# Kernel tuning notes

Measured on AMD Instinct MI355X. Metric: run time of the kernel, lower is better.

Reference implementation:

```python
import jax, jax.numpy as jnp
import numpy as np

N_BASIS = 8
CUTOFF = 5.0
NORM_FACTOR = 16.0


def setup_inputs() -> dict:
    key = jax.random.key(0)
    ks = jax.random.split(key, 10)
    N, E, C = 20000, 320000, 32
    s = 1.0 / np.sqrt(C)
    return {
        "node0": jax.random.normal(ks[0], (N, C), jnp.float32),
        "node1": jax.random.normal(ks[1], (N, C, 3), jnp.float32),
        "node2": jax.random.normal(ks[2], (N, C, 3, 3), jnp.float32),
        "rij": jax.random.normal(ks[3], (E, 3), jnp.float32) * 1.5,
        "Wrad": jax.random.normal(ks[4], (11, N_BASIS, C), jnp.float32) * 0.3,
        "U": jax.random.normal(ks[5], (3, C, C), jnp.float32) * s,
        "V": jax.random.normal(ks[6], (8, C, C), jnp.float32) * s,
        "Wg": jax.random.normal(ks[7], (3, C, C), jnp.float32) * s,
        "idx_i": jax.random.randint(ks[8], (E,), 0, N),
        "idx_j": jax.random.randint(ks[9], (E,), 0, N),
    }


def reference(node0, node1, node2, rij, Wrad, U, V, Wg, idx_i, idx_j):
    N, C = node0.shape
    # radial basis (Gaussian RBF * cosine cutoff envelope)
    dist = jnp.sqrt(jnp.sum(rij * rij, -1) + 1e-12)           # [E]
    rhat = rij / dist[:, None]                                 # [E,3]
    centers = jnp.linspace(0.5, CUTOFF, N_BASIS, dtype=node0.dtype)
    fc = 0.5 * (jnp.cos(jnp.pi * jnp.clip(dist / CUTOFF, 0.0, 1.0)) + 1.0)
    rbf = jnp.exp(-4.0 * (dist[:, None] - centers) ** 2) * fc[:, None]  # [E,B]
    # per-coupling-path radial filters: 11 paths (in_way, r_way, out_way)
    w = jnp.einsum('eb,pbc->pec', rbf, Wrad)                   # [11,E,C]
    # gather neighbor (node_j) features per edge
    g0 = node0[idx_j]                                          # [E,C]
    g1 = node1[idx_j]                                          # [E,C,3]
    g2 = node2[idx_j]                                          # [E,C,3,3]
    m1 = rhat                                                  # [E,3]
    m2 = rhat[:, :, None] * rhat[:, None, :]                   # [E,3,3]
    # graph conv: contract node_j tensor with r-way moment, weighted by radial filter
    # paths: 0:(0,0,0) 1:(0,1,1) 2:(0,2,2) 3:(1,0,1) 4:(1,1,0) 5:(1,1,2)
    #        6:(1,2,1) 7:(2,0,2) 8:(2,1,1) 9:(2,2,0) 10:(2,2,2)
    msg0 = (g0 * w[0]
            + jnp.einsum('eca,ea->ec', g1, m1) * w[4]
            + jnp.einsum('ecab,eab->ec', g2, m2) * w[9])
    msg1 = (jnp.einsum('ec,ea->eca', g0 * w[1], m1)
            + g1 * w[3][:, :, None]
            + jnp.einsum('eca,eab->ecb', g1, m2) * w[6][:, :, None]
            + jnp.einsum('ecab,eb->eca', g2, m1) * w[8][:, :, None])
    msg2 = (jnp.einsum('ec,eab->ecab', g0 * w[2], m2)
            + jnp.einsum('eca,eb->ecab', g1 * w[5][:, :, None], m1)
            + g2 * w[7][:, :, None, None]
            + jnp.einsum('ecab,ebd->ecad', g2, m2) * w[10][:, :, None, None])
    # scatter_add aggregation into per-atom features, normalized
    a0 = jax.ops.segment_sum(msg0, idx_i, num_segments=N) / NORM_FACTOR
    a1 = jax.ops.segment_sum(msg1, idx_i, num_segments=N) / NORM_FACTOR
    a2 = jax.ops.segment_sum(msg2, idx_i, num_segments=N) / NORM_FACTOR
    # multi-body self-interaction (2-body linear U + 3-body products V)
    y0 = (jnp.einsum('nc,cd->nd', a0, U[0])
          + jnp.einsum('nc,cd->nd', a0 * a0, V[0])
          + jnp.einsum('nc,cd->nd', jnp.einsum('nca,nca->nc', a1, a1), V[3])
          + jnp.einsum('nc,cd->nd', jnp.einsum('ncab,ncab->nc', a2, a2), V[6]))
    y1 = (jnp.einsum('nca,cd->nda', a1, U[1])
          + jnp.einsum('nca,cd->nda', a0[:, :, None] * a1, V[1])
          + jnp.einsum('nca,cd->nda', jnp.einsum('nca,ncab->ncb', a1, a2), V[5]))
    y2 = (jnp.einsum('ncab,cd->ndab', a2, U[2])
          + jnp.einsum('ncab,cd->ndab', a0[:, :, None, None] * a2, V[2])
          + jnp.einsum('ncab,cd->ndab', a1[:, :, :, None] * a1[:, :, None, :], V[4])
          + jnp.einsum('ncab,cd->ndab', jnp.einsum('ncab,ncbd->ncad', a2, a2), V[7]))
    # gated nonlinearity (scalar channel gates tensor ways) + residual add
    new0 = node0 + jax.nn.silu(y0 @ Wg[0])
    new1 = node1 + y1 * jax.nn.silu(y0 @ Wg[1])[:, :, None]
    new2 = node2 + y2 * jax.nn.silu(y0 @ Wg[2])[:, :, None, None]
    return (new0, new1, new2)
```

## Files before the change

### kernel.cpp

```cpp
#include <hip/hip_runtime.h>
#include <hip/hip_fp16.h>

#define NCH 32
#define NB 8
#define NPB 8

typedef __attribute__((ext_vector_type(2))) _Float16 half2r;

__device__ __forceinline__ unsigned short f2h(float f) {
    return __half_as_ushort(__float2half_rn(f));
}
__device__ __forceinline__ float h2f_lo(unsigned int u) {
    half2r v = __builtin_bit_cast(half2r, u);
    return (float)v.x;
}
__device__ __forceinline__ float h2f_hi(unsigned int u) {
    half2r v = __builtin_bit_cast(half2r, u);
    return (float)v.y;
}

__device__ __forceinline__ float fdot2u(unsigned int a, unsigned int b, float c) {
#if __has_builtin(__builtin_amdgcn_fdot2)
    return __builtin_amdgcn_fdot2(__builtin_bit_cast(half2r, a),
                                  __builtin_bit_cast(half2r, b), c, false);
#else
    half2r av = __builtin_bit_cast(half2r, a);
    half2r bv = __builtin_bit_cast(half2r, b);
    return c + (float)av.x * (float)bv.x + (float)av.y * (float)bv.y;
#endif
}

__device__ __forceinline__ void acc8h(float& y, uint4 w, uint4 f) {
    y = fdot2u(w.x, f.x, y);
    y = fdot2u(w.y, f.y, y);
    y = fdot2u(w.z, f.z, y);
    y = fdot2u(w.w, f.w, y);
}
__device__ __forceinline__ void acc8fh(float& y, uint4 w, float4 a, float4 b) {
    y += h2f_lo(w.x) * a.x + h2f_hi(w.x) * a.y + h2f_lo(w.y) * a.z + h2f_hi(w.y) * a.w
       + h2f_lo(w.z) * b.x + h2f_hi(w.z) * b.y + h2f_lo(w.w) * b.z + h2f_hi(w.w) * b.w;
}

__global__ __launch_bounds__(256) void wprep_kernel(
    const float* __restrict__ U, const float* __restrict__ V,
    const float* __restrict__ Wg, const float* __restrict__ Wrad,
    unsigned short* __restrict__ wswz, unsigned int* __restrict__ wradp)
{
    int idx = blockIdx.x * 256 + threadIdx.x;
    if (idx < 14 * 1024) {
        int m = idx >> 10, r = idx & 1023;
        int c = r >> 5, d = r & 31;
        float v;
        if (m < 3)       v = U[m * 1024 + c * 32 + d];
        else if (m < 11) v = V[(m - 3) * 1024 + c * 32 + d];
        else             v = Wg[(m - 11) * 1024 + c * 32 + d];
        wswz[m * 1024 + (c >> 3) * 256 + d * 8 + (c & 7)] = f2h(v);
    } else {
        int k = idx - 14 * 1024;
        if (k < 11 * 4 * 32) {
            int c = k & 31, bb = (k >> 5) & 3, p = k >> 7;
            float lo = Wrad[p * 256 + (2 * bb) * 32 + c] * (1.0f / 16.0f);
            float hi = Wrad[p * 256 + (2 * bb + 1) * 32 + c] * (1.0f / 16.0f);
            wradp[(p * 4 + bb) * 32 + c] =
                (unsigned int)f2h(lo) | ((unsigned int)f2h(hi) << 16);
        }
    }
}

__global__ __launch_bounds__(256) void hist_kernel(
    const int* __restrict__ idx_i, int* __restrict__ counts, int E)
{
    int e = blockIdx.x * 256 + threadIdx.x;
    if (e < E) atomicAdd(&counts[idx_i[e]], 1);
}

__global__ __launch_bounds__(256) void scan_reduce_kernel(
    const int* __restrict__ counts, int* __restrict__ blocksums, int N)
{
    const int tid = threadIdx.x;
    const int base = blockIdx.x * 1024;
    int v = 0;
    #pragma unroll
    for (int k = 0; k < 4; ++k) {
        int i = base + tid * 4 + k;
        if (i < N) v += counts[i];
    }
    #pragma unroll
    for (int off = 1; off < 64; off <<= 1) v += __shfl_xor(v, off, 64);
    __shared__ int wsum[4];
    if ((tid & 63) == 0) wsum[tid >> 6] = v;
    __syncthreads();
    if (tid == 0) blocksums[blockIdx.x] = wsum[0] + wsum[1] + wsum[2] + wsum[3];
}

__global__ void scan_top_kernel(
    const int* __restrict__ blocksums, int* __restrict__ bases,
    int* __restrict__ offsets, int nb, int N)
{
    int l = threadIdx.x;
    int v = (l < nb) ? blocksums[l] : 0;
    int incl = v;
    #pragma unroll
    for (int off = 1; off < 64; off <<= 1) {
        int t = __shfl_up(incl, off, 64);
        if (l >= off) incl += t;
    }
    if (l < nb) bases[l] = incl - v;
    if (l == nb - 1) offsets[N] = incl;
}

__global__ __launch_bounds__(256) void scan_write_kernel(
    int* __restrict__ cursor, const int* __restrict__ bases,
    int* __restrict__ offsets, int N)
{
    const int tid = threadIdx.x;
    const int i0 = blockIdx.x * 1024 + tid * 4;
    int v[4]; int lsum = 0;
    #pragma unroll
    for (int k = 0; k < 4; ++k) {
        int i = i0 + k;
        v[k] = (i < N) ? cursor[i] : 0;
        lsum += v[k];
    }
    int incl = lsum;
    #pragma unroll
    for (int off = 1; off < 64; off <<= 1) {
        int t = __shfl_up(incl, off, 64);
        if ((tid & 63) >= off) incl += t;
    }
    __shared__ int wsum[4];
    if ((tid & 63) == 63) wsum[tid >> 6] = incl;
    __syncthreads();
    int add = bases[blockIdx.x];
    for (int w = 0; w < (tid >> 6); ++w) add += wsum[w];
    int run = add + incl - lsum;
    #pragma unroll
    for (int k = 0; k < 4; ++k) {
        int i = i0 + k;
        if (i < N) { offsets[i] = run; cursor[i] = run; run += v[k]; }
    }
}

__global__ __launch_bounds__(256) void scatter_meta_kernel(
    const int* __restrict__ idx_i, const int* __restrict__ idx_j,
    const float* __restrict__ rij, int* __restrict__ cursor,
    int* __restrict__ jord, float4* __restrict__ meta2, int E)
{
    int e = blockIdx.x * 256 + threadIdx.x;
    if (e >= E) return;
    float rx = rij[3 * e + 0], ry = rij[3 * e + 1], rz = rij[3 * e + 2];
    float dist = sqrtf(rx * rx + ry * ry + rz * rz + 1e-12f);
    float inv = 1.0f / dist;
    float tcl = fminf(dist * 0.2f, 1.0f);
    float fc = 0.5f * (cosf(3.14159265358979f * tcl) + 1.0f);
    float rbf[NB];
    #pragma unroll
    for (int b = 0; b < NB; ++b) {
        float dd = dist - (0.5f + (float)b * (4.5f / 7.0f));
        rbf[b] = expf(-4.0f * dd * dd) * fc;
    }
    unsigned int rb01 = (unsigned int)f2h(rbf[0]) | ((unsigned int)f2h(rbf[1]) << 16);
    unsigned int rb23 = (unsigned int)f2h(rbf[2]) | ((unsigned int)f2h(rbf[3]) << 16);
    unsigned int rb45 = (unsigned int)f2h(rbf[4]) | ((unsigned int)f2h(rbf[5]) << 16);
    unsigned int rb67 = (unsigned int)f2h(rbf[6]) | ((unsigned int)f2h(rbf[7]) << 16);
    int slot = atomicAdd(&cursor[idx_i[e]], 1);
    jord[slot] = idx_j[e];
    meta2[2 * slot + 0] = make_float4(rx * inv, ry * inv, rz * inv, __uint_as_float(rb01));
    meta2[2 * slot + 1] = make_float4(__uint_as_float(rb23), __uint_as_float(rb45),
                                      __uint_as_float(rb67), 0.0f);
}

__global__ __launch_bounds__(256) void transpose_nodes_kernel(
    const float* __restrict__ node0, const float* __restrict__ node1,
    const float* __restrict__ node2, unsigned short* __restrict__ n0h,
    unsigned short* __restrict__ n1h, unsigned short* __restrict__ n2h, int N)
{
    int n = blockIdx.x * 8 + (threadIdx.x >> 5);
    int c = threadIdx.x & 31;
    if (n >= N) return;
    n0h[n * 32 + c] = f2h(node0[n * 32 + c]);
    #pragma unroll
    for (int a = 0; a < 3; ++a) n1h[n * 96 + a * 32 + c] = f2h(node1[n * 96 + c * 3 + a]);
    #pragma unroll
    for (int k = 0; k < 9; ++k) n2h[n * 288 + k * 32 + c] = f2h(node2[n * 288 + c * 9 + k]);
}

__global__ __launch_bounds__(256, 4) void aggregate_kernel(
    const unsigned short* __restrict__ n0h, const unsigned short* __restrict__ n1h,
    const unsigned short* __restrict__ n2h, const unsigned int* __restrict__ wradp,
    const int* __restrict__ jord, const float4* __restrict__ meta2,
    const int* __restrict__ offsets,
    float* __restrict__ a0, float* __restrict__ a1, float* __restrict__ a2,
    int N)
{
    const int c = threadIdx.x & 31;
    const int g = threadIdx.x >> 5;
    const int n = blockIdx.x * NPB + g;
    if (n >= N) return;

    unsigned int wr[11][4];
    #pragma unroll
    for (int p = 0; p < 11; ++p)
        #pragma unroll
        for (int bb = 0; bb < 4; ++bb)
            wr[p][bb] = wradp[(p * 4 + bb) * 32 + c];

    const int beg = offsets[n], end = offsets[n + 1];

    float A0 = 0.f;
    float A1[3] = {0.f, 0.f, 0.f};
    float A2[9] = {0.f, 0.f, 0.f, 0.f, 0.f, 0.f, 0.f, 0.f, 0.f};

    float4 M0n = make_float4(0.f, 0.f, 0.f, 0.f), M1n = M0n;
    unsigned short G0n = 0, G1n[3] = {0, 0, 0}, G2n[9] = {};

    int s = beg;
    if (s < end) {
        int j = jord[s];
        M0n = meta2[2 * s + 0]; M1n = meta2[2 * s + 1];
        G0n = n0h[j * 32 + c];
        #pragma unroll
        for (int a = 0; a < 3; ++a) G1n[a] = n1h[j * 96 + a * 32 + c];
        #pragma unroll
        for (int k = 0; k < 9; ++k) G2n[k] = n2h[j * 288 + k * 32 + c];
    }

    while (s < end) {
        float4 M0 = M0n, M1 = M1n;
        float G0 = __half2float(__ushort_as_half(G0n));
        float G1[3], G2[9];
        #pragma unroll
        for (int a = 0; a < 3; ++a) G1[a] = __half2float(__ushort_as_half(G1n[a]));
        #pragma unroll
        for (int k = 0; k < 9; ++k) G2[k] = __half2float(__ushort_as_half(G2n[k]));

        int sn = s + 1;
        if (sn < end) {
            int j = jord[sn];
            M0n = meta2[2 * sn + 0]; M1n = meta2[2 * sn + 1];
            G0n = n0h[j * 32 + c];
            #pragma unroll
            for (int a = 0; a < 3; ++a) G1n[a] = n1h[j * 96 + a * 32 + c];
            #pragma unroll
            for (int k = 0; k < 9; ++k) G2n[k] = n2h[j * 288 + k * 32 + c];
        }

        float h[3] = { M0.x, M0.y, M0.z };
        unsigned int rb01 = __float_as_uint(M0.w);
        unsigned int rb23 = __float_as_uint(M1.x);
        unsigned int rb45 = __float_as_uint(M1.y);
        unsigned int rb67 = __float_as_uint(M1.z);

        float w[11];
        #pragma unroll
        for (int p = 0; p < 11; ++p)
            w[p] = fdot2u(rb01, wr[p][0],
                   fdot2u(rb23, wr[p][1],
                   fdot2u(rb45, wr[p][2],
                   fdot2u(rb67, wr[p][3], 0.0f))));

        float s1 = G1[0] * h[0] + G1[1] * h[1] + G1[2] * h[2];
        float tt[3];
        #pragma unroll
        for (int a = 0; a < 3; ++a)
            tt[a] = G2[a * 3 + 0] * h[0] + G2[a * 3 + 1] * h[1] + G2[a * 3 + 2] * h[2];
        float s2 = tt[0] * h[0] + tt[1] * h[1] + tt[2] * h[2];

        A0 += G0 * w[0] + s1 * w[4] + s2 * w[9];
        #pragma unroll
        for (int a = 0; a < 3; ++a)
            A1[a] += (G0 * w[1] + s1 * w[6]) * h[a] + G1[a] * w[3] + tt[a] * w[8];
        #pragma unroll
        for (int a = 0; a < 3; ++a) {
            float pre = G0 * w[2] * h[a] + G1[a] * w[5] + tt[a] * w[10];
            #pragma unroll
            for (int b = 0; b < 3; ++b)
                A2[a * 3 + b] += pre * h[b] + G2[a * 3 + b] * w[7];
        }
        s = sn;
    }

    a0[n * 32 + c] = A0;
    #pragma unroll
    for (int a = 0; a < 3; ++a) a1[n * 96 + a * 32 + c] = A1[a];
    #pragma unroll
    for (int k = 0; k < 9; ++k) a2[n * 288 + k * 32 + c] = A2[k];
}

__global__ __launch_bounds__(256) void node_kernel(
    const float* __restrict__ node0, const float* __restrict__ node1,
    const float* __restrict__ node2, const unsigned short* __restrict__ wswz,
    float* __restrict__ out0, float* __restrict__ out1, float* __restrict__ out2,
    int N)
{
    __shared__ alignas(16) unsigned short wT[14 * 1024];
    __shared__ alignas(16) unsigned short feat[NPB * 49 * 32];
    __shared__ alignas(16) float y0s[NPB][32];

    {
        const uint4* src = reinterpret_cast<const uint4*>(wswz);
        uint4* dst = reinterpret_cast<uint4*>(wT);
        for (int i = threadIdx.x; i < 14 * 128; i += 256) dst[i] = src[i];
    }

    const int g = threadIdx.x >> 5;
    const int lane = threadIdx.x & 31;
    const int n = blockIdx.x * NPB + g;
    const bool active = (n < N);

    if (active) {
        const int c = lane;
        float A0 = out0[n * 32 + c];
        float A1[3], A2[9];
        #pragma unroll
        for (int a = 0; a < 3; ++a) A1[a] = out1[n * 96 + a * 32 + c];
        #pragma unroll
        for (int k = 0; k < 9; ++k) A2[k] = out2[n * 288 + k * 32 + c];

        unsigned short* F = &feat[g * 49 * 32];
        F[0 * 32 + c] = f2h(A0);
        F[1 * 32 + c] = f2h(A0 * A0);
        F[2 * 32 + c] = f2h(A1[0] * A1[0] + A1[1] * A1[1] + A1[2] * A1[2]);
        float n2 = 0.f;
        #pragma unroll
        for (int k = 0; k < 9; ++k) n2 += A2[k] * A2[k];
        F[3 * 32 + c] = f2h(n2);
        #pragma unroll
        for (int a = 0; a < 3; ++a) {
            F[(4 + a) * 32 + c] = f2h(A1[a]);
            F[(7 + a) * 32 + c] = f2h(A0 * A1[a]);
        }
        #pragma unroll
        for (int b = 0; b < 3; ++b) {
            float s = A1[0] * A2[0 * 3 + b] + A1[1] * A2[1 * 3 + b] + A1[2] * A2[2 * 3 + b];
            F[(10 + b) * 32 + c] = f2h(s);
        }
        #pragma unroll
        for (int k = 0; k < 9; ++k) {
            F[(13 + k) * 32 + c] = f2h(A2[k]);
            F[(22 + k) * 32 + c] = f2h(A0 * A2[k]);
        }
        #pragma unroll
        for (int a = 0; a < 3; ++a)
            #pragma unroll
            for (int b = 0; b < 3; ++b)
                F[(31 + a * 3 + b) * 32 + c] = f2h(A1[a] * A1[b]);
        #pragma unroll
        for (int a = 0; a < 3; ++a)
            #pragma unroll
            for (int dd = 0; dd < 3; ++dd) {
                float s = A2[a * 3 + 0] * A2[0 * 3 + dd] + A2[a * 3 + 1] * A2[1 * 3 + dd]
                        + A2[a * 3 + 2] * A2[2 * 3 + dd];
                F[(40 + a * 3 + dd) * 32 + c] = f2h(s);
            }
    }
    __syncthreads();

    const int d = lane;
    float y0v = 0.f;
    float y1v[3] = {0.f, 0.f, 0.f};
    float y2v[9] = {0.f, 0.f, 0.f, 0.f, 0.f, 0.f, 0.f, 0.f, 0.f};

    if (active) {
        const uint4* W4 = reinterpret_cast<const uint4*>(wT);
        const uint4* F4 = reinterpret_cast<const uint4*>(&feat[g * 49 * 32]);
        for (int q = 0; q < 4; ++q) {
            const int q32d = q * 32 + d;
            acc8h(y0v, W4[0 * 128 + q32d], F4[0 * 4 + q]);
            acc8h(y0v, W4[3 * 128 + q32d], F4[1 * 4 + q]);
            acc8h(y0v, W4[6 * 128 + q32d], F4[2 * 4 + q]);
            acc8h(y0v, W4[9 * 128 + q32d], F4[3 * 4 + q]);
            uint4 wU1 = W4[1 * 128 + q32d];
            uint4 wV1 = W4[4 * 128 + q32d];
            uint4 wV5 = W4[8 * 128 + q32d];
            #pragma unroll
            for (int a = 0; a < 3; ++a) {
                acc8h(y1v[a], wU1, F4[(4 + a) * 4 + q]);
                acc8h(y1v[a], wV1, F4[(7 + a) * 4 + q]);
                acc8h(y1v[a], wV5, F4[(10 + a) * 4 + q]);
            }
            uint4 wU2 = W4[2 * 128 + q32d];
            uint4 wV2 = W4[5 * 128 + q32d];
            uint4 wV4 = W4[7 * 128 + q32d];
            uint4 wV7 = W4[10 * 128 + q32d];
            #pragma unroll
            for (int k = 0; k < 9; ++k) {
                acc8h(y2v[k], wU2, F4[(13 + k) * 4 + q]);
                acc8h(y2v[k], wV2, F4[(22 + k) * 4 + q]);
                acc8h(y2v[k], wV4, F4[(31 + k) * 4 + q]);
                acc8h(y2v[k], wV7, F4[(40 + k) * 4 + q]);
            }
        }
        y0s[g][d] = y0v;
    }
    __syncthreads();

    if (!active) return;

    float t0 = 0.f, t1 = 0.f, t2 = 0.f;
    {
        const uint4* W4 = reinterpret_cast<const uint4*>(wT);
        const float4* Y4 = reinterpret_cast<const float4*>(y0s[g]);
        #pragma unroll
        for (int q = 0; q < 4; ++q) {
            const int q32d = q * 32 + d;
            float4 ya = Y4[2 * q], yb = Y4[2 * q + 1];
            acc8fh(t0, W4[11 * 128 + q32d], ya, yb);
            acc8fh(t1, W4[12 * 128 + q32d], ya, yb);
            acc8fh(t2, W4[13 * 128 + q32d], ya, yb);
        }
    }
    float s0 = t0 / (1.0f + expf(-t0));
    float s1 = t1 / (1.0f + expf(-t1));
    float s2 = t2 / (1.0f + expf(-t2));

    out0[n * 32 + d] = node0[n * 32 + d] + s0;
    #pragma unroll
    for (int a = 0; a < 3; ++a)
        out1[n * 96 + d * 3 + a] = node1[n * 96 + d * 3 + a] + y1v[a] * s1;
    #pragma unroll
    for (int k = 0; k < 9; ++k)
        out2[n * 288 + d * 9 + k] = node2[n * 288 + d * 9 + k] + y2v[k] * s2;
}

extern "C" void kernel_launch(void* const* d_in, const int* in_sizes, int n_in,
                              void* d_out, int out_size, void* d_ws, size_t ws_size,
                              hipStream_t stream)
{
    const float* node0 = (const float*)d_in[0];
    const float* node1 = (const float*)d_in[1];
    const float* node2 = (const float*)d_in[2];
    const float* rij   = (const float*)d_in[3];
    const float* Wrad  = (const float*)d_in[4];
    const float* U     = (const float*)d_in[5];
    const float* V     = (const float*)d_in[6];
    const float* Wg    = (const float*)d_in[7];
    const int* idx_i   = (const int*)d_in[8];
    const int* idx_j   = (const int*)d_in[9];

    const int N = in_sizes[0] / 32;
    const int E = in_sizes[3] / 3;

    float* out0 = (float*)d_out;
    float* out1 = out0 + (size_t)N * 32;
    float* out2 = out1 + (size_t)N * 96;

    size_t off = 0;
    auto walloc = [&](size_t bytes) -> void* {
        off = (off + 63) & ~(size_t)63;
        void* p = (char*)d_ws + off;
        off += bytes;
        return p;
    };
    int*    cursor    = (int*)   walloc((size_t)N * 4);
    int*    offsets   = (int*)   walloc((size_t)(N + 1) * 4);
    int*    blocksums = (int*)   walloc(64 * 4);
    int*    bases     = (int*)   walloc(64 * 4);
    int*    jord      = (int*)   walloc((size_t)E * 4);
    float4* meta2     = (float4*)walloc((size_t)E * 2 * sizeof(float4));
    unsigned short* n0h = (unsigned short*)walloc((size_t)N * 32 * 2);
    unsigned short* n1h = (unsigned short*)walloc((size_t)N * 96 * 2);
    unsigned short* n2h = (unsigned short*)walloc((size_t)N * 288 * 2);
    unsigned short* wswz = (unsigned short*)walloc(14 * 1024 * 2);
    unsigned int*  wradp = (unsigned int*)walloc(11 * 4 * 32 * 4);
    (void)ws_size;

    const int nb = (N + 1023) / 1024;

    hipMemsetAsync(cursor, 0, (size_t)N * sizeof(int), stream);

    wprep_kernel<<<dim3((14 * 1024 + 11 * 4 * 32 + 255) / 256), dim3(256), 0, stream>>>(
        U, V, Wg, Wrad, wswz, wradp);
    hist_kernel<<<dim3((E + 255) / 256), dim3(256), 0, stream>>>(idx_i, cursor, E);
    scan_reduce_kernel<<<dim3(nb), dim3(256), 0, stream>>>(cursor, blocksums, N);
    scan_top_kernel<<<dim3(1), dim3(64), 0, stream>>>(blocksums, bases, offsets, nb, N);
    scan_write_kernel<<<dim3(nb), dim3(256), 0, stream>>>(cursor, bases, offsets, N);
    scatter_meta_kernel<<<dim3((E + 255) / 256), dim3(256), 0, stream>>>(
        idx_i, idx_j, rij, cursor, jord, meta2, E);
    transpose_nodes_kernel<<<dim3((N + 7) / 8), dim3(256), 0, stream>>>(
        node0, node1, node2, n0h, n1h, n2h, N);

    aggregate_kernel<<<dim3((N + NPB - 1) / NPB), dim3(256), 0, stream>>>(
        n0h, n1h, n2h, wradp, jord, meta2, offsets, out0, out1, out2, N);

    node_kernel<<<dim3((N + NPB - 1) / NPB), dim3(256), 0, stream>>>(
        node0, node1, node2, wswz, out0, out1, out2, N);
}
```

Baseline: 285.2 us.

## Pack per-node fp16 features into 32-byte records, single-block scan, smaller aggregate blocks

Node features are packed per (node, channel) into one contiguous 32-byte record of 13 fp16 values plus padding. The gather in the aggregation loop therefore becomes two 16-byte vector loads instead of thirteen scattered 2-byte loads. The three-kernel prefix scan is merged into one 1024-thread single-block kernel, which removes two launches. The aggregate kernel now runs 64-thread blocks covering two nodes each, which should improve load balance across uneven degrees. The padding adds about 23% more bytes per gathered row, and the serial per-thread scan loop is a small latency cost.

```diff
diff --git a/kernel.cpp b/kernel.cpp
--- a/kernel.cpp
+++ b/kernel.cpp
@@ -74,71 +74,41 @@
     if (e < E) atomicAdd(&counts[idx_i[e]], 1);
 }
 
-__global__ __launch_bounds__(256) void scan_reduce_kernel(
-    const int* __restrict__ counts, int* __restrict__ blocksums, int N)
+__global__ __launch_bounds__(1024) void scan_kernel(
+    int* __restrict__ cursor ,
+    int* __restrict__ offsets, int N)
 {
     const int tid = threadIdx.x;
-    const int base = blockIdx.x * 1024;
-    int v = 0;
-    #pragma unroll
-    for (int k = 0; k < 4; ++k) {
-        int i = base + tid * 4 + k;
-        if (i < N) v += counts[i];
-    }
-    #pragma unroll
-    for (int off = 1; off < 64; off <<= 1) v += __shfl_xor(v, off, 64);
-    __shared__ int wsum[4];
-    if ((tid & 63) == 0) wsum[tid >> 6] = v;
-    __syncthreads();
-    if (tid == 0) blocksums[blockIdx.x] = wsum[0] + wsum[1] + wsum[2] + wsum[3];
-}
-
-__global__ void scan_top_kernel(
-    const int* __restrict__ blocksums, int* __restrict__ bases,
-    int* __restrict__ offsets, int nb, int N)
-{
-    int l = threadIdx.x;
-    int v = (l < nb) ? blocksums[l] : 0;
-    int incl = v;
+    const int lane = tid & 63, wid = tid >> 6;
+    const int per = (N + 1023) / 1024;
+    const int i0 = tid * per;
+    const int i1 = min(i0 + per, N);
+
+    int lsum = 0;
+    for (int i = i0; i < i1; ++i) lsum += cursor[i];
+
+    int incl = lsum;
     #pragma unroll
     for (int off = 1; off < 64; off <<= 1) {
         int t = __shfl_up(incl, off, 64);
-        if (l >= off) incl += t;
-    }
-    if (l < nb) bases[l] = incl - v;
-    if (l == nb - 1) offsets[N] = incl;
-}
-
-__global__ __launch_bounds__(256) void scan_write_kernel(
-    int* __restrict__ cursor, const int* __restrict__ bases,
-    int* __restrict__ offsets, int N)
-{
-    const int tid = threadIdx.x;
-    const int i0 = blockIdx.x * 1024 + tid * 4;
-    int v[4]; int lsum = 0;
-    #pragma unroll
-    for (int k = 0; k < 4; ++k) {
-        int i = i0 + k;
-        v[k] = (i < N) ? cursor[i] : 0;
-        lsum += v[k];
-    }
-    int incl = lsum;
-    #pragma unroll
-    for (int off = 1; off < 64; off <<= 1) {
-        int t = __shfl_up(incl, off, 64);
-        if ((tid & 63) >= off) incl += t;
-    }
-    __shared__ int wsum[4];
-    if ((tid & 63) == 63) wsum[tid >> 6] = incl;
+        if (lane >= off) incl += t;
+    }
+    __shared__ int wsums[16], wbase[16];
+    if (lane == 63) wsums[wid] = incl;
     __syncthreads();
-    int add = bases[blockIdx.x];
-    for (int w = 0; w < (tid >> 6); ++w) add += wsum[w];
-    int run = add + incl - lsum;
-    #pragma unroll
-    for (int k = 0; k < 4; ++k) {
-        int i = i0 + k;
-        if (i < N) { offsets[i] = run; cursor[i] = run; run += v[k]; }
-    }
+    if (tid == 0) {
+        int acc = 0;
+        #pragma unroll
+        for (int k = 0; k < 16; ++k) { int t = wsums[k]; wbase[k] = acc; acc += t; }
+    }
+    __syncthreads();
+
+    int run = wbase[wid] + incl - lsum;
+    for (int i = i0; i < i1; ++i) {
+        int cv = cursor[i];
+        offsets[i] = run; cursor[i] = run; run += cv;
+    }
+    if (tid == 1023) offsets[N] = wbase[15] + incl;
 }
 
 __global__ __launch_bounds__(256) void scatter_meta_kernel(
@@ -170,24 +140,31 @@
                                       __uint_as_float(rb67), 0.0f);
 }
 
-__global__ __launch_bounds__(256) void transpose_nodes_kernel(
+__global__ __launch_bounds__(256) void pack_nodes_kernel(
     const float* __restrict__ node0, const float* __restrict__ node1,
-    const float* __restrict__ node2, unsigned short* __restrict__ n0h,
-    unsigned short* __restrict__ n1h, unsigned short* __restrict__ n2h, int N)
+    const float* __restrict__ node2, uint4* __restrict__ pk, int N)
 {
     int n = blockIdx.x * 8 + (threadIdx.x >> 5);
     int c = threadIdx.x & 31;
     if (n >= N) return;
-    n0h[n * 32 + c] = f2h(node0[n * 32 + c]);
-    #pragma unroll
-    for (int a = 0; a < 3; ++a) n1h[n * 96 + a * 32 + c] = f2h(node1[n * 96 + c * 3 + a]);
-    #pragma unroll
-    for (int k = 0; k < 9; ++k) n2h[n * 288 + k * 32 + c] = f2h(node2[n * 288 + c * 9 + k]);
-}
-
-__global__ __launch_bounds__(256, 4) void aggregate_kernel(
-    const unsigned short* __restrict__ n0h, const unsigned short* __restrict__ n1h,
-    const unsigned short* __restrict__ n2h, const unsigned int* __restrict__ wradp,
+    unsigned short r[16];
+    r[0] = f2h(node0[n * 32 + c]);
+    #pragma unroll
+    for (int a = 0; a < 3; ++a) r[1 + a] = f2h(node1[n * 96 + c * 3 + a]);
+    #pragma unroll
+    for (int k = 0; k < 9; ++k) r[4 + k] = f2h(node2[n * 288 + c * 9 + k]);
+    r[13] = r[14] = r[15] = 0;
+    unsigned int u[8];
+    #pragma unroll
+    for (int i = 0; i < 8; ++i)
+        u[i] = (unsigned int)r[2 * i] | ((unsigned int)r[2 * i + 1] << 16);
+    uint4* dst = pk + (size_t)n * 64 + c * 2;
+    dst[0] = make_uint4(u[0], u[1], u[2], u[3]);
+    dst[1] = make_uint4(u[4], u[5], u[6], u[7]);
+}
+
+__global__ __launch_bounds__(64) void aggregate_kernel(
+    const uint4* __restrict__ pk, const unsigned int* __restrict__ wradp,
     const int* __restrict__ jord, const float4* __restrict__ meta2,
     const int* __restrict__ offsets,
     float* __restrict__ a0, float* __restrict__ a1, float* __restrict__ a2,
@@ -195,7 +172,7 @@
 {
     const int c = threadIdx.x & 31;
     const int g = threadIdx.x >> 5;
-    const int n = blockIdx.x * NPB + g;
+    const int n = blockIdx.x * 2 + g;
     if (n >= N) return;
 
     unsigned int wr[11][4];
@@ -212,38 +189,33 @@
     float A2[9] = {0.f, 0.f, 0.f, 0.f, 0.f, 0.f, 0.f, 0.f, 0.f};
 
     float4 M0n = make_float4(0.f, 0.f, 0.f, 0.f), M1n = M0n;
-    unsigned short G0n = 0, G1n[3] = {0, 0, 0}, G2n[9] = {};
+    uint4 Q0n = make_uint4(0, 0, 0, 0), Q1n = Q0n;
 
     int s = beg;
     if (s < end) {
         int j = jord[s];
         M0n = meta2[2 * s + 0]; M1n = meta2[2 * s + 1];
-        G0n = n0h[j * 32 + c];
-        #pragma unroll
-        for (int a = 0; a < 3; ++a) G1n[a] = n1h[j * 96 + a * 32 + c];
-        #pragma unroll
-        for (int k = 0; k < 9; ++k) G2n[k] = n2h[j * 288 + k * 32 + c];
+        const uint4* P = pk + (size_t)j * 64 + c * 2;
+        Q0n = P[0]; Q1n = P[1];
     }
 
     while (s < end) {
         float4 M0 = M0n, M1 = M1n;
-        float G0 = __half2float(__ushort_as_half(G0n));
-        float G1[3], G2[9];
-        #pragma unroll
-        for (int a = 0; a < 3; ++a) G1[a] = __half2float(__ushort_as_half(G1n[a]));
-        #pragma unroll
-        for (int k = 0; k < 9; ++k) G2[k] = __half2float(__ushort_as_half(G2n[k]));
+        uint4 Q0 = Q0n, Q1 = Q1n;
 
         int sn = s + 1;
         if (sn < end) {
             int j = jord[sn];
             M0n = meta2[2 * sn + 0]; M1n = meta2[2 * sn + 1];
-            G0n = n0h[j * 32 + c];
-            #pragma unroll
-            for (int a = 0; a < 3; ++a) G1n[a] = n1h[j * 96 + a * 32 + c];
-            #pragma unroll
-            for (int k = 0; k < 9; ++k) G2n[k] = n2h[j * 288 + k * 32 + c];
-        }
+            const uint4* P = pk + (size_t)j * 64 + c * 2;
+            Q0n = P[0]; Q1n = P[1];
+        }
+
+        float G0    = h2f_lo(Q0.x);
+        float G1[3] = { h2f_hi(Q0.x), h2f_lo(Q0.y), h2f_hi(Q0.y) };
+        float G2[9] = { h2f_lo(Q0.z), h2f_hi(Q0.z), h2f_lo(Q0.w), h2f_hi(Q0.w),
+                        h2f_lo(Q1.x), h2f_hi(Q1.x), h2f_lo(Q1.y), h2f_hi(Q1.y),
+                        h2f_lo(Q1.z) };
 
         float h[3] = { M0.x, M0.y, M0.z };
         unsigned int rb01 = __float_as_uint(M0.w);
@@ -454,34 +426,26 @@
     };
     int*    cursor    = (int*)   walloc((size_t)N * 4);
     int*    offsets   = (int*)   walloc((size_t)(N + 1) * 4);
-    int*    blocksums = (int*)   walloc(64 * 4);
-    int*    bases     = (int*)   walloc(64 * 4);
     int*    jord      = (int*)   walloc((size_t)E * 4);
     float4* meta2     = (float4*)walloc((size_t)E * 2 * sizeof(float4));
-    unsigned short* n0h = (unsigned short*)walloc((size_t)N * 32 * 2);
-    unsigned short* n1h = (unsigned short*)walloc((size_t)N * 96 * 2);
-    unsigned short* n2h = (unsigned short*)walloc((size_t)N * 288 * 2);
+    uint4*  pk        = (uint4*) walloc((size_t)N * 1024);
     unsigned short* wswz = (unsigned short*)walloc(14 * 1024 * 2);
     unsigned int*  wradp = (unsigned int*)walloc(11 * 4 * 32 * 4);
     (void)ws_size;
 
-    const int nb = (N + 1023) / 1024;
-
     hipMemsetAsync(cursor, 0, (size_t)N * sizeof(int), stream);
 
     wprep_kernel<<<dim3((14 * 1024 + 11 * 4 * 32 + 255) / 256), dim3(256), 0, stream>>>(
         U, V, Wg, Wrad, wswz, wradp);
     hist_kernel<<<dim3((E + 255) / 256), dim3(256), 0, stream>>>(idx_i, cursor, E);
-    scan_reduce_kernel<<<dim3(nb), dim3(256), 0, stream>>>(cursor, blocksums, N);
-    scan_top_kernel<<<dim3(1), dim3(64), 0, stream>>>(blocksums, bases, offsets, nb, N);
-    scan_write_kernel<<<dim3(nb), dim3(256), 0, stream>>>(cursor, bases, offsets, N);
+    scan_kernel<<<dim3(1), dim3(1024), 0, stream>>>(cursor, offsets, N);
     scatter_meta_kernel<<<dim3((E + 255) / 256), dim3(256), 0, stream>>>(
         idx_i, idx_j, rij, cursor, jord, meta2, E);
-    transpose_nodes_kernel<<<dim3((N + 7) / 8), dim3(256), 0, stream>>>(
-        node0, node1, node2, n0h, n1h, n2h, N);
-
-    aggregate_kernel<<<dim3((N + NPB - 1) / NPB), dim3(256), 0, stream>>>(
-        n0h, n1h, n2h, wradp, jord, meta2, offsets, out0, out1, out2, N);
+    pack_nodes_kernel<<<dim3((N + 7) / 8), dim3(256), 0, stream>>>(
+        node0, node1, node2, pk, N);
+
+    aggregate_kernel<<<dim3((N + 1) / 2), dim3(64), 0, stream>>>(
+        pk, wradp, jord, meta2, offsets, out0, out1, out2, N);
 
     node_kernel<<<dim3((N + NPB - 1) / NPB), dim3(256), 0, stream>>>(
         node0, node1, node2, wswz, out0, out1, out2, N);
```

New measurement: 304.6 us. 1.07x slower.
